# Optimization experiments

Hardware: AMD Instinct MI355X
Metric: run time of the kernel (lower is better)

Reference implementation:

```python
import jax, jax.numpy as jnp
import numpy as np

BATCH, SEQ, EMBED = 4, 4096, 512
NUM_HEADS = 8
D_K = EMBED // NUM_HEADS  # = n_wires of the quantum layer


def setup_inputs() -> dict:
    key = jax.random.key(0)
    k1, k2, k3, k4 = jax.random.split(key, 4)
    x = jax.random.normal(k1, (BATCH, SEQ, EMBED), dtype=jnp.float32)
    theta = jax.random.normal(k2, (D_K,), dtype=jnp.float32)          # trainable RX angles (shared across heads)
    W_out = jax.random.normal(k3, (EMBED, EMBED), dtype=jnp.float32) * (1.0 / np.sqrt(EMBED))
    b_out = jax.random.normal(k4, (EMBED,), dtype=jnp.float32) * 0.01
    return {"x": x, "theta": theta, "W_out": W_out, "b_out": b_out}


def reference(x, theta, W_out, b_out):
    b, s, e = x.shape
    d_k = theta.shape[0]
    h = e // d_k
    # Quantum stage: per wire, RX(x_i) then RX(theta_i) on |0>, measure PauliZ.
    # RX gates on the same wire compose, and <Z| RX(phi)|0> state> = cos(phi),
    # so the whole per-head circuit is elementwise cos(x + theta).
    xh = x.reshape(b, s, h, d_k)                 # split heads
    q_concat = jnp.cos(xh + theta).reshape(b, s, e)
    # q = k = v = out_proj(q_concat)  (same Linear applied three times)
    q = q_concat @ W_out.T + b_out               # [b, s, e]
    scale = 1.0 / jnp.sqrt(jnp.asarray(d_k, dtype=q.dtype))
    scores = jax.nn.softmax(jnp.einsum('bie,bje->bij', q, q) * scale, axis=-1)  # [b, s, s]
    out = jnp.einsum('bij,bje->bie', scores, q)  # dropout = identity (inference)
    return out
```

## Files before the change

### kernel.cpp

```cpp
#include <hip/hip_runtime.h>

typedef __bf16 bf16_t;
typedef bf16_t bf16x8 __attribute__((ext_vector_type(8)));
typedef bf16_t bf16x4 __attribute__((ext_vector_type(4)));
typedef float f32x4 __attribute__((ext_vector_type(4)));

#define BATCH 4
#define SEQ 4096
#define EMBED 512
#define MTOT (BATCH * SEQ)
#define BC 32
#define FITERS (SEQ / BC)

__device__ bf16_t Wbf_g[EMBED * EMBED];

__device__ __forceinline__ void async_copy16(const bf16_t* g, bf16_t* l) {
    __builtin_amdgcn_global_load_lds(
        (const __attribute__((address_space(1))) unsigned int*)g,
        (__attribute__((address_space(3))) unsigned int*)l, 16, 0, 0);
}

__global__ __launch_bounds__(256) void cvt_w_kernel(const float* __restrict__ W) {
    const int i = (blockIdx.x * 256 + threadIdx.x) * 4;
    float4 v = *(const float4*)&W[i];
    bf16x4 o;
    o[0] = (bf16_t)v.x; o[1] = (bf16_t)v.y; o[2] = (bf16_t)v.z; o[3] = (bf16_t)v.w;
    *(bf16x4*)&Wbf_g[i] = o;
}

__global__ __launch_bounds__(256) void cvt_a_kernel(
    const float* __restrict__ x, const float* __restrict__ theta,
    bf16_t* __restrict__ abuf)
{
    const int i = (blockIdx.x * 256 + threadIdx.x) * 8;
    float4 a = *(const float4*)&x[i];
    float4 b = *(const float4*)&x[i + 4];
    const int e0 = i & 63;
    bf16x8 o;
    o[0] = (bf16_t)__cosf(a.x + theta[e0 + 0]);
    o[1] = (bf16_t)__cosf(a.y + theta[e0 + 1]);
    o[2] = (bf16_t)__cosf(a.z + theta[e0 + 2]);
    o[3] = (bf16_t)__cosf(a.w + theta[e0 + 3]);
    o[4] = (bf16_t)__cosf(b.x + theta[e0 + 4]);
    o[5] = (bf16_t)__cosf(b.y + theta[e0 + 5]);
    o[6] = (bf16_t)__cosf(b.z + theta[e0 + 6]);
    o[7] = (bf16_t)__cosf(b.w + theta[e0 + 7]);
    *(bf16x8*)&abuf[i] = o;
}

__global__ __launch_bounds__(256, 2) void gemm_q_kernel(
    const bf16_t* __restrict__ abuf, const float* __restrict__ bias,
    bf16_t* __restrict__ kperm, bf16_t* __restrict__ qt)
{
    __shared__ alignas(16) bf16_t smem[4 * 8192];

    const int t    = threadIdx.x;
    const int lane = t & 63;
    const int wave = t >> 6;
    const int l15  = lane & 15;
    const int quad = lane >> 4;
    const int m0   = (blockIdx.x >> 2) * 128;
    const int n0   = (blockIdx.x & 3) * 128;
    const int wm   = wave >> 1;
    const int wn   = wave & 1;

    const int drow = lane >> 3;
    const int dseg = lane & 7;
    const int sseg = dseg ^ drow;

    f32x4 acc[4][4];
#pragma unroll
    for (int mt = 0; mt < 4; ++mt)
#pragma unroll
        for (int nt = 0; nt < 4; ++nt) acc[mt][nt] = (f32x4){0.f, 0.f, 0.f, 0.f};

    auto stage = [&](int buf, int k0) {
        bf16_t* As = smem + buf * 16384;
        bf16_t* Bs = As + 8192;
#pragma unroll
        for (int j = 0; j < 4; ++j) {
            const int c   = wave * 4 + j;
            const int row = c * 8 + drow;
            async_copy16(&abuf[(size_t)(m0 + row) * 512 + k0 + sseg * 8], &As[c * 512]);
            async_copy16(&Wbf_g[(size_t)(n0 + row) * 512 + k0 + sseg * 8], &Bs[c * 512]);
        }
    };

    stage(0, 0);
    __syncthreads();
    int cur = 0;
    for (int kk = 0; kk < 8; ++kk) {
        if (kk + 1 < 8) stage(cur ^ 1, (kk + 1) * 64);
        const bf16_t* As = smem + cur * 16384;
        const bf16_t* Bs = As + 8192;
#pragma unroll
        for (int kh = 0; kh < 2; ++kh) {
            bf16x8 af[4], bfr[4];
#pragma unroll
            for (int i = 0; i < 4; ++i) {
                const int rA = wm * 64 + i * 16 + l15;
                const int rB = wn * 64 + i * 16 + l15;
                const int sg = kh * 4 + quad;
                af[i]  = *(const bf16x8*)&As[rA * 64 + (sg ^ (rA & 7)) * 8];
                bfr[i] = *(const bf16x8*)&Bs[rB * 64 + (sg ^ (rB & 7)) * 8];
            }
#pragma unroll
            for (int mt = 0; mt < 4; ++mt)
#pragma unroll
                for (int nt = 0; nt < 4; ++nt)
                    acc[mt][nt] = __builtin_amdgcn_mfma_f32_16x16x32_bf16(af[mt], bfr[nt], acc[mt][nt], 0, 0, 0);
        }
        __syncthreads();
        cur ^= 1;
    }

    const int b     = m0 >> 12;
    const int mloc  = m0 & 4095;
    bf16_t* Es = smem;

#pragma unroll
    for (int nt = 0; nt < 4; ++nt) {
        const int colL = wn * 64 + nt * 16 + l15;
        const float bv = bias[n0 + colL];
        const int kfL = colL >> 5;
        const int inc = ((colL >> 3) & 3) * 128 + (colL & 7);
#pragma unroll
        for (int mt = 0; mt < 4; ++mt) {
            const int rowL0 = wm * 64 + mt * 16 + quad * 4;
            const int c     = (rowL0 >> 5) * 8 + ((rowL0 >> 4) & 1) * 4 + kfL;
            const int base  = c * 512 + inc + (rowL0 & 15) * 8;
#pragma unroll
            for (int r = 0; r < 4; ++r)
                Es[base + r * 8] = (bf16_t)(acc[mt][nt][r] + bv);
        }
    }
    __syncthreads();
    {
        const int tileB = mloc >> 5;
        const int kfB   = n0 >> 5;
#pragma unroll
        for (int p = 0; p < 8; ++p) {
            const int flat = p * 256 + t;
            const int c2   = flat >> 6;
            const int off  = (flat & 63) * 8;
            const int tile = c2 >> 3;
            const int mh   = (c2 >> 2) & 1;
            const int kfL2 = c2 & 3;
            const size_t dst = (size_t)b * (SEQ * EMBED)
                             + (size_t)(tileB + tile) * 16384
                             + (size_t)(mh * 16 + kfB + kfL2) * 512 + off;
            *(bf16x8*)&kperm[dst] = *(const bf16x8*)&Es[c2 * 512 + off];
        }
    }
    __syncthreads();
#pragma unroll
    for (int nt = 0; nt < 4; ++nt) {
        const int colL = wn * 64 + nt * 16 + l15;
        const float bv = bias[n0 + colL];
#pragma unroll
        for (int mt = 0; mt < 4; ++mt) {
            const int rowL0 = wm * 64 + mt * 16 + quad * 4;
#pragma unroll
            for (int r = 0; r < 4; ++r)
                Es[colL * 136 + rowL0 + r] = (bf16_t)(acc[mt][nt][r] + bv);
        }
    }
    __syncthreads();
    {
#pragma unroll
        for (int p = 0; p < 8; ++p) {
            const int flat = p * 256 + t;
            const int col  = flat >> 4;
            const int sub  = flat & 15;
            *(bf16x8*)&qt[((size_t)(b * 512 + n0 + col) << 12) + mloc + sub * 8]
                = *(const bf16x8*)&Es[col * 136 + sub * 8];
        }
    }
}

__global__ __launch_bounds__(512, 2) void flash_kernel(
    const bf16_t* __restrict__ kp, const bf16_t* __restrict__ qt,
    float* __restrict__ out)
{
    __shared__ alignas(16) bf16_t Ks[2][32 * 512];
    __shared__ alignas(16) bf16_t Ps[2][4 * 512];
    __shared__ float Ls[8][16];
    __shared__ float Lf[64];

    const int t    = threadIdx.x;
    const int lane = t & 63;
    const int w    = t >> 6;
    const int l15  = lane & 15;
    const int quad = lane >> 4;
    const int qg   = w >> 1;
    const int ktw  = w & 1;

    const int L      = blockIdx.x;
    const int xcd    = L & 7;
    const int slot   = L >> 3;
    const int batch  = xcd >> 1;
    const int qtile  = (xcd & 1) * 32 + slot;

    const int q0 = qtile * 64;
    const bf16_t* kpb = kp + (size_t)batch * SEQ * EMBED;
    const bf16_t* qtb = qt + (size_t)batch * EMBED * SEQ;

#pragma unroll
    for (int cc = 0; cc < 4; ++cc) {
        const int f = cc * 8 + w;
        async_copy16(&kpb[(size_t)f * 512 + lane * 8], &Ks[0][f * 512]);
    }

    bf16x8 bQ[16];
    {
        const size_t qb = (size_t)(qtile * 2 + (qg >> 1)) * 16384
                        + (size_t)(qg & 1) * 16 * 512;
#pragma unroll
        for (int kf = 0; kf < 16; ++kf)
            bQ[kf] = *(const bf16x8*)&kpb[qb + kf * 512 + lane * 8];
    }

    f32x4 O[4][4];
#pragma unroll
    for (int m = 0; m < 4; ++m)
#pragma unroll
        for (int n = 0; n < 4; ++n) O[m][n] = (f32x4){0.f, 0.f, 0.f, 0.f};
    float lpart = 0.f;

    for (int it = 0; it < FITERS; ++it) {
        const int cbuf = it & 1;
        const int pbuf = cbuf ^ 1;
        __syncthreads();
        bf16x8 bv[4];
        if (it) {
            const int kv = (it - 1) * BC;
#pragma unroll
            for (int n = 0; n < 4; ++n)
                bv[n] = *(const bf16x8*)&qtb[(size_t)(w * 64 + n * 16 + l15) * 4096
                                             + kv + quad * 8];
        }
        if (it + 1 < FITERS) {
#pragma unroll
            for (int cc = 0; cc < 4; ++cc) {
                const int f = cc * 8 + w;
                async_copy16(&kpb[(size_t)(it + 1) * 16384 + f * 512 + lane * 8],
                             &Ks[pbuf][f * 512]);
            }
        }
        f32x4 s;
        {
            f32x4 a0 = (f32x4){0.f, 0.f, 0.f, 0.f};
            f32x4 a1 = (f32x4){0.f, 0.f, 0.f, 0.f};
#pragma unroll
            for (int kf = 0; kf < 8; ++kf) {
                bf16x8 ak0 = *(const bf16x8*)&Ks[cbuf][(ktw * 16 + kf) * 512 + lane * 8];
                bf16x8 ak1 = *(const bf16x8*)&Ks[cbuf][(ktw * 16 + 8 + kf) * 512 + lane * 8];
                a0 = __builtin_amdgcn_mfma_f32_16x16x32_bf16(ak0, bQ[kf],     a0, 0, 0, 0);
                a1 = __builtin_amdgcn_mfma_f32_16x16x32_bf16(ak1, bQ[8 + kf], a1, 0, 0, 0);
            }
            s = a0 + a1;
        }
        {
            bf16x4 pk;
#pragma unroll
            for (int r = 0; r < 4; ++r) {
                bf16_t pb = (bf16_t)__expf(s[r] * 0.125f);
                lpart += (float)pb;
                pk[r] = pb;
            }
            *(bf16x4*)&Ps[cbuf][qg * 512 + (ktw * 2 + (quad >> 1)) * 128
                                + l15 * 8 + (quad & 1) * 4] = pk;
        }
        if (it) {
            bf16x8 pa[4];
#pragma unroll
            for (int mt = 0; mt < 4; ++mt)
                pa[mt] = *(const bf16x8*)&Ps[pbuf][mt * 512 + lane * 8];
            __builtin_amdgcn_s_setprio(1);
#pragma unroll
            for (int n = 0; n < 4; ++n)
#pragma unroll
                for (int mt = 0; mt < 4; ++mt)
                    O[mt][n] = __builtin_amdgcn_mfma_f32_16x16x32_bf16(pa[mt], bv[n], O[mt][n], 0, 0, 0);
            __builtin_amdgcn_s_setprio(0);
        }
    }
    __syncthreads();
    {
        const int pbuf = (FITERS - 1) & 1;
        const int kv = (FITERS - 1) * BC;
        bf16x8 bv[4];
#pragma unroll
        for (int n = 0; n < 4; ++n)
            bv[n] = *(const bf16x8*)&qtb[(size_t)(w * 64 + n * 16 + l15) * 4096
                                         + kv + quad * 8];
        bf16x8 pa[4];
#pragma unroll
        for (int mt = 0; mt < 4; ++mt)
            pa[mt] = *(const bf16x8*)&Ps[pbuf][mt * 512 + lane * 8];
        __builtin_amdgcn_s_setprio(1);
#pragma unroll
        for (int n = 0; n < 4; ++n)
#pragma unroll
            for (int mt = 0; mt < 4; ++mt)
                O[mt][n] = __builtin_amdgcn_mfma_f32_16x16x32_bf16(pa[mt], bv[n], O[mt][n], 0, 0, 0);
        __builtin_amdgcn_s_setprio(0);
    }

    {
        float ls = lpart;
        ls += __shfl_xor(ls, 16);
        ls += __shfl_xor(ls, 32);
        if (lane < 16) Ls[w][lane] = ls;
    }
    __syncthreads();
    if (t < 64)
        Lf[t] = 1.0f / (Ls[(t >> 4) * 2][t & 15] + Ls[(t >> 4) * 2 + 1][t & 15]);
    __syncthreads();

#pragma unroll
    for (int mt = 0; mt < 4; ++mt)
#pragma unroll
        for (int r = 0; r < 4; ++r) {
            const int qloc = mt * 16 + quad * 4 + r;
            const float inv = Lf[qloc];
            const size_t row = (size_t)batch * SEQ + q0 + qloc;
#pragma unroll
            for (int n = 0; n < 4; ++n)
                __builtin_nontemporal_store(O[mt][n][r] * inv,
                    &out[row * 512 + w * 64 + n * 16 + l15]);
        }
}

extern "C" void kernel_launch(void* const* d_in, const int* in_sizes, int n_in,
                              void* d_out, int out_size, void* d_ws, size_t ws_size,
                              hipStream_t stream) {
    const float* x     = (const float*)d_in[0];
    const float* theta = (const float*)d_in[1];
    const float* W     = (const float*)d_in[2];
    const float* bias  = (const float*)d_in[3];
    float* out    = (float*)d_out;
    bf16_t* kperm = (bf16_t*)d_ws;
    bf16_t* qt    = kperm + (size_t)MTOT * EMBED;
    bf16_t* abuf  = qt + (size_t)MTOT * EMBED;

    cvt_w_kernel<<<dim3(EMBED * EMBED / 4 / 256), dim3(256), 0, stream>>>(W);

    cvt_a_kernel<<<dim3(MTOT * EMBED / 8 / 256), dim3(256), 0, stream>>>(x, theta, abuf);

    gemm_q_kernel<<<dim3((MTOT / 128) * 4), dim3(256), 0, stream>>>(abuf, bias, kperm, qt);

    flash_kernel<<<dim3(SEQ / 64 * BATCH), dim3(512), 0, stream>>>(kperm, qt, out);
}
```

Before: 339.0 us.

## Warp-specialize flash kernel into score producers and PV consumers with 32-row tiles

Splits the flash attention block into four producer waves that compute QK^T scores and exp into shared memory, and four consumer waves that read P and V to accumulate the output. The query tile shrinks from 64 to 32 rows, doubling the grid, and the occupancy hint rises to 4 blocks per CU. The aim is to overlap the score MFMAs with the PV MFMAs and to raise parallelism. In exchange, each K tile is now reused by half as many queries, so K traffic per output doubles. Producers and consumers must also stay in lockstep through matching __syncthreads counts.

```diff
diff --git a/kernel.cpp b/kernel.cpp
--- a/kernel.cpp
+++ b/kernel.cpp
@@ -178,77 +178,61 @@
     }
 }
 
-__global__ __launch_bounds__(512, 2) void flash_kernel(
+__global__ __launch_bounds__(512, 4) void flash_kernel(
     const bf16_t* __restrict__ kp, const bf16_t* __restrict__ qt,
     float* __restrict__ out)
 {
     __shared__ alignas(16) bf16_t Ks[2][32 * 512];
-    __shared__ alignas(16) bf16_t Ps[2][4 * 512];
-    __shared__ float Ls[8][16];
-    __shared__ float Lf[64];
+    __shared__ alignas(16) bf16_t Ps[2][2 * 512];
+    __shared__ float Ls[4][16];
+    __shared__ float Lf[32];
 
     const int t    = threadIdx.x;
     const int lane = t & 63;
     const int w    = t >> 6;
     const int l15  = lane & 15;
     const int quad = lane >> 4;
-    const int qg   = w >> 1;
-    const int ktw  = w & 1;
 
     const int L      = blockIdx.x;
     const int xcd    = L & 7;
     const int slot   = L >> 3;
     const int batch  = xcd >> 1;
-    const int qtile  = (xcd & 1) * 32 + slot;
-
-    const int q0 = qtile * 64;
+    const int qtile  = (xcd & 1) * 64 + slot;
+
+    const int q0 = qtile * 32;
     const bf16_t* kpb = kp + (size_t)batch * SEQ * EMBED;
     const bf16_t* qtb = qt + (size_t)batch * EMBED * SEQ;
 
-#pragma unroll
-    for (int cc = 0; cc < 4; ++cc) {
-        const int f = cc * 8 + w;
-        async_copy16(&kpb[(size_t)f * 512 + lane * 8], &Ks[0][f * 512]);
-    }
-
-    bf16x8 bQ[16];
-    {
-        const size_t qb = (size_t)(qtile * 2 + (qg >> 1)) * 16384
-                        + (size_t)(qg & 1) * 16 * 512;
-#pragma unroll
-        for (int kf = 0; kf < 16; ++kf)
-            bQ[kf] = *(const bf16x8*)&kpb[qb + kf * 512 + lane * 8];
-    }
-
-    f32x4 O[4][4];
-#pragma unroll
-    for (int m = 0; m < 4; ++m)
-#pragma unroll
-        for (int n = 0; n < 4; ++n) O[m][n] = (f32x4){0.f, 0.f, 0.f, 0.f};
-    float lpart = 0.f;
-
-    for (int it = 0; it < FITERS; ++it) {
-        const int cbuf = it & 1;
-        const int pbuf = cbuf ^ 1;
-        __syncthreads();
-        bf16x8 bv[4];
-        if (it) {
-            const int kv = (it - 1) * BC;
-#pragma unroll
-            for (int n = 0; n < 4; ++n)
-                bv[n] = *(const bf16x8*)&qtb[(size_t)(w * 64 + n * 16 + l15) * 4096
-                                             + kv + quad * 8];
-        }
-        if (it + 1 < FITERS) {
-#pragma unroll
-            for (int cc = 0; cc < 4; ++cc) {
-                const int f = cc * 8 + w;
-                async_copy16(&kpb[(size_t)(it + 1) * 16384 + f * 512 + lane * 8],
-                             &Ks[pbuf][f * 512]);
-            }
-        }
-        f32x4 s;
+    if (w < 4) {
+        const int qg  = w >> 1;
+        const int ktw = w & 1;
+
+#pragma unroll
+        for (int cc = 0; cc < 8; ++cc) {
+            const int f = cc * 4 + w;
+            async_copy16(&kpb[(size_t)f * 512 + lane * 8], &Ks[0][f * 512]);
+        }
+        bf16x8 bQ[16];
         {
+            const size_t qb = (size_t)qtile * 16384 + (size_t)qg * 16 * 512;
+#pragma unroll
+            for (int kf = 0; kf < 16; ++kf)
+                bQ[kf] = *(const bf16x8*)&kpb[qb + kf * 512 + lane * 8];
+        }
+        float lpart = 0.f;
+
+        for (int it = 0; it < FITERS; ++it) {
+            const int cbuf = it & 1;
+            const int pbuf = cbuf ^ 1;
+            __syncthreads();
+            if (it + 1 < FITERS) {
+#pragma unroll
+                for (int cc = 0; cc < 8; ++cc) {
+                    const int f = cc * 4 + w;
+                    async_copy16(&kpb[(size_t)(it + 1) * 16384 + f * 512 + lane * 8],
+                                 &Ks[pbuf][f * 512]);
+                }
+            }
             f32x4 a0 = (f32x4){0.f, 0.f, 0.f, 0.f};
             f32x4 a1 = (f32x4){0.f, 0.f, 0.f, 0.f};
 #pragma unroll
@@ -258,9 +242,7 @@
                 a0 = __builtin_amdgcn_mfma_f32_16x16x32_bf16(ak0, bQ[kf],     a0, 0, 0, 0);
                 a1 = __builtin_amdgcn_mfma_f32_16x16x32_bf16(ak1, bQ[8 + kf], a1, 0, 0, 0);
             }
-            s = a0 + a1;
-        }
-        {
+            f32x4 s = a0 + a1;
             bf16x4 pk;
 #pragma unroll
             for (int r = 0; r < 4; ++r) {
@@ -271,65 +253,90 @@
             *(bf16x4*)&Ps[cbuf][qg * 512 + (ktw * 2 + (quad >> 1)) * 128
                                 + l15 * 8 + (quad & 1) * 4] = pk;
         }
-        if (it) {
-            bf16x8 pa[4];
-#pragma unroll
-            for (int mt = 0; mt < 4; ++mt)
+        {
+            float ls = lpart;
+            ls += __shfl_xor(ls, 16);
+            ls += __shfl_xor(ls, 32);
+            if (lane < 16) Ls[w][lane] = ls;
+        }
+        __syncthreads();
+        if (t < 32)
+            Lf[t] = 1.0f / (Ls[(t >> 4) * 2][t & 15] + Ls[(t >> 4) * 2 + 1][t & 15]);
+        __syncthreads();
+    } else {
+        const int pw = w - 4;
+        f32x4 O[2][8];
+#pragma unroll
+        for (int m = 0; m < 2; ++m)
+#pragma unroll
+            for (int n = 0; n < 8; ++n) O[m][n] = (f32x4){0.f, 0.f, 0.f, 0.f};
+
+        for (int it = 0; it < FITERS; ++it) {
+            __syncthreads();
+            if (it) {
+                const int pbuf = (it & 1) ^ 1;
+                const int kv = (it - 1) * BC;
+                bf16x8 pa[2];
+#pragma unroll
+                for (int mt = 0; mt < 2; ++mt)
+                    pa[mt] = *(const bf16x8*)&Ps[pbuf][mt * 512 + lane * 8];
+#pragma unroll
+                for (int nh = 0; nh < 2; ++nh) {
+                    bf16x8 bv[4];
+#pragma unroll
+                    for (int j = 0; j < 4; ++j)
+                        bv[j] = *(const bf16x8*)&qtb[(size_t)(pw * 128 + (nh * 4 + j) * 16 + l15) * 4096
+                                                     + kv + quad * 8];
+                    __builtin_amdgcn_s_setprio(1);
+#pragma unroll
+                    for (int j = 0; j < 4; ++j)
+#pragma unroll
+                        for (int mt = 0; mt < 2; ++mt)
+                            O[mt][nh * 4 + j] = __builtin_amdgcn_mfma_f32_16x16x32_bf16(
+                                pa[mt], bv[j], O[mt][nh * 4 + j], 0, 0, 0);
+                    __builtin_amdgcn_s_setprio(0);
+                }
+            }
+        }
+        __syncthreads();
+        {
+            const int pbuf = (FITERS - 1) & 1;
+            const int kv = (FITERS - 1) * BC;
+            bf16x8 pa[2];
+#pragma unroll
+            for (int mt = 0; mt < 2; ++mt)
                 pa[mt] = *(const bf16x8*)&Ps[pbuf][mt * 512 + lane * 8];
-            __builtin_amdgcn_s_setprio(1);
-#pragma unroll
-            for (int n = 0; n < 4; ++n)
-#pragma unroll
-                for (int mt = 0; mt < 4; ++mt)
-                    O[mt][n] = __builtin_amdgcn_mfma_f32_16x16x32_bf16(pa[mt], bv[n], O[mt][n], 0, 0, 0);
-            __builtin_amdgcn_s_setprio(0);
-        }
-    }
-    __syncthreads();
-    {
-        const int pbuf = (FITERS - 1) & 1;
-        const int kv = (FITERS - 1) * BC;
-        bf16x8 bv[4];
-#pragma unroll
-        for (int n = 0; n < 4; ++n)
-            bv[n] = *(const bf16x8*)&qtb[(size_t)(w * 64 + n * 16 + l15) * 4096
-                                         + kv + quad * 8];
-        bf16x8 pa[4];
-#pragma unroll
-        for (int mt = 0; mt < 4; ++mt)
-            pa[mt] = *(const bf16x8*)&Ps[pbuf][mt * 512 + lane * 8];
-        __builtin_amdgcn_s_setprio(1);
-#pragma unroll
-        for (int n = 0; n < 4; ++n)
-#pragma unroll
-            for (int mt = 0; mt < 4; ++mt)
-                O[mt][n] = __builtin_amdgcn_mfma_f32_16x16x32_bf16(pa[mt], bv[n], O[mt][n], 0, 0, 0);
-        __builtin_amdgcn_s_setprio(0);
-    }
-
-    {
-        float ls = lpart;
-        ls += __shfl_xor(ls, 16);
-        ls += __shfl_xor(ls, 32);
-        if (lane < 16) Ls[w][lane] = ls;
-    }
-    __syncthreads();
-    if (t < 64)
-        Lf[t] = 1.0f / (Ls[(t >> 4) * 2][t & 15] + Ls[(t >> 4) * 2 + 1][t & 15]);
-    __syncthreads();
-
-#pragma unroll
-    for (int mt = 0; mt < 4; ++mt)
-#pragma unroll
-        for (int r = 0; r < 4; ++r) {
-            const int qloc = mt * 16 + quad * 4 + r;
-            const float inv = Lf[qloc];
-            const size_t row = (size_t)batch * SEQ + q0 + qloc;
-#pragma unroll
-            for (int n = 0; n < 4; ++n)
-                __builtin_nontemporal_store(O[mt][n][r] * inv,
-                    &out[row * 512 + w * 64 + n * 16 + l15]);
-        }
+#pragma unroll
+            for (int nh = 0; nh < 2; ++nh) {
+                bf16x8 bv[4];
+#pragma unroll
+                for (int j = 0; j < 4; ++j)
+                    bv[j] = *(const bf16x8*)&qtb[(size_t)(pw * 128 + (nh * 4 + j) * 16 + l15) * 4096
+                                                 + kv + quad * 8];
+                __builtin_amdgcn_s_setprio(1);
+#pragma unroll
+                for (int j = 0; j < 4; ++j)
+#pragma unroll
+                    for (int mt = 0; mt < 2; ++mt)
+                        O[mt][nh * 4 + j] = __builtin_amdgcn_mfma_f32_16x16x32_bf16(
+                            pa[mt], bv[j], O[mt][nh * 4 + j], 0, 0, 0);
+                __builtin_amdgcn_s_setprio(0);
+            }
+        }
+        __syncthreads();
+#pragma unroll
+        for (int mt = 0; mt < 2; ++mt)
+#pragma unroll
+            for (int r = 0; r < 4; ++r) {
+                const int qloc = mt * 16 + quad * 4 + r;
+                const float inv = Lf[qloc];
+                const size_t row = (size_t)batch * SEQ + q0 + qloc;
+#pragma unroll
+                for (int n = 0; n < 8; ++n)
+                    __builtin_nontemporal_store(O[mt][n][r] * inv,
+                        &out[row * 512 + pw * 128 + n * 16 + l15]);
+            }
+    }
 }
 
 extern "C" void kernel_launch(void* const* d_in, const int* in_sizes, int n_in,
@@ -350,5 +357,5 @@
 
     gemm_q_kernel<<<dim3((MTOT / 128) * 4), dim3(256), 0, stream>>>(abuf, bias, kperm, qt);
 
-    flash_kernel<<<dim3(SEQ / 64 * BATCH), dim3(512), 0, stream>>>(kperm, qt, out);
-}
+    flash_kernel<<<dim3(SEQ / 32 * BATCH), dim3(512), 0, stream>>>(kperm, qt, out);
+}
```

New measurement: 400.1 us. 1.18x slower.
